# Kernel tuning notes

Hardware: AMD Instinct MI355X
Metric: run time of the kernel (lower is better)

Reference implementation:

```python
import jax, jax.numpy as jnp
import numpy as np

N_NODES = 100000
N_EDGES = 3200000
D_IN = 256
D_OUT = 256


def setup_inputs() -> dict:
    key = jax.random.key(0)
    k1, k2, k3, k4, k5, k6 = jax.random.split(key, 6)
    x = jax.random.normal(k1, (N_NODES, D_IN), dtype=jnp.float32)
    adj_row = jnp.sort(jax.random.randint(k2, (N_EDGES,), 0, N_NODES, dtype=jnp.int64))
    adj_col = jax.random.randint(k3, (N_EDGES,), 0, N_NODES, dtype=jnp.int64)
    adj_val = jax.random.uniform(k4, (N_EDGES,), dtype=jnp.float32)
    stdv = 1.0 / np.sqrt(D_OUT)
    weight = jax.random.uniform(k5, (D_IN, D_OUT), dtype=jnp.float32, minval=-stdv, maxval=stdv)
    bias = jax.random.uniform(k6, (D_OUT,), dtype=jnp.float32, minval=-stdv, maxval=stdv)
    return {"x": x, "adj_row": adj_row, "adj_col": adj_col, "adj_val": adj_val,
            "weight": weight, "bias": bias}


def reference(x, adj_row, adj_col, adj_val, weight, bias):
    # support = x @ W   -> [N, D_OUT]
    support = x @ weight
    # output = spmm(adj, support): gather source rows, scale by edge value,
    # segment-reduce into destination rows.
    msgs = adj_val[:, None] * support[adj_col]          # [E, D_OUT]
    output = jax.ops.segment_sum(msgs, adj_row, num_segments=N_NODES)
    return output + bias
```

## Files before the change

kernel.cpp:

```cpp
#include <hip/hip_runtime.h>
#include <hip/hip_bf16.h>

#define D_FEAT 256

typedef __attribute__((ext_vector_type(8))) __bf16 bf16x8;
typedef __attribute__((ext_vector_type(4))) __bf16 bf16x4;
typedef __attribute__((ext_vector_type(4))) float f32x4;

__global__ __launch_bounds__(256) void cast_wt(
    const float* __restrict__ W, __bf16* __restrict__ Wt) {
  const int n = blockIdx.x;
  const int k = threadIdx.x;
  Wt[n * 256 + k] = (__bf16)W[k * 256 + n];
}

#define APITCH 40

__global__ __launch_bounds__(256) void gemm_mfma(
    const float* __restrict__ X, const __bf16* __restrict__ Wt,
    __bf16* __restrict__ S, int M) {
  __shared__ __bf16 As[128 * APITCH];
  __shared__ __bf16 Bs[64 * APITCH];
  const int tid = threadIdx.x;
  const int wave = tid >> 6;
  const int lane = tid & 63;
  const int m0 = blockIdx.x * 128;
  const int n0 = blockIdx.y * 64;

  f32x4 acc[2][4] = {};

  const int l15 = lane & 15;
  const int kh8 = (lane >> 4) * 8;

  for (int k0 = 0; k0 < D_FEAT; k0 += 32) {
    {
      const int r = tid >> 1;
      const int kh = (tid & 1) * 16;
      const int gr = m0 + r;
      float v[16];
      if (gr < M) {
        const float* src = X + (size_t)gr * D_FEAT + k0 + kh;
#pragma unroll
        for (int q = 0; q < 4; ++q) {
          float4 f = *reinterpret_cast<const float4*>(src + q * 4);
          v[q * 4 + 0] = f.x; v[q * 4 + 1] = f.y;
          v[q * 4 + 2] = f.z; v[q * 4 + 3] = f.w;
        }
      } else {
#pragma unroll
        for (int q = 0; q < 16; ++q) v[q] = 0.f;
      }
      bf16x8 b0, b1;
#pragma unroll
      for (int q = 0; q < 8; ++q) { b0[q] = (__bf16)v[q]; b1[q] = (__bf16)v[q + 8]; }
      *reinterpret_cast<bf16x8*>(&As[r * APITCH + kh]) = b0;
      *reinterpret_cast<bf16x8*>(&As[r * APITCH + kh + 8]) = b1;
    }
    {
      const int nr = tid >> 2;
      const int q = (tid & 3) * 8;
      bf16x8 b = *reinterpret_cast<const bf16x8*>(
          Wt + (size_t)(n0 + nr) * D_FEAT + k0 + q);
      *reinterpret_cast<bf16x8*>(&Bs[nr * APITCH + q]) = b;
    }
    __syncthreads();

    bf16x8 a[2], b[4];
#pragma unroll
    for (int rg = 0; rg < 2; ++rg)
      a[rg] = *reinterpret_cast<const bf16x8*>(
          &As[(wave * 32 + rg * 16 + l15) * APITCH + kh8]);
#pragma unroll
    for (int cg = 0; cg < 4; ++cg)
      b[cg] = *reinterpret_cast<const bf16x8*>(
          &Bs[(cg * 16 + l15) * APITCH + kh8]);
#pragma unroll
    for (int rg = 0; rg < 2; ++rg)
#pragma unroll
      for (int cg = 0; cg < 4; ++cg)
        acc[rg][cg] = __builtin_amdgcn_mfma_f32_16x16x32_bf16(
            a[rg], b[cg], acc[rg][cg], 0, 0, 0);
    __syncthreads();
  }

#pragma unroll
  for (int rg = 0; rg < 2; ++rg) {
    const int rbase = m0 + wave * 32 + rg * 16 + (lane >> 4) * 4;
#pragma unroll
    for (int cg = 0; cg < 4; ++cg) {
      const int c = n0 + cg * 16 + l15;
#pragma unroll
      for (int r = 0; r < 4; ++r) {
        const int row = rbase + r;
        if (row < M) S[(size_t)row * D_FEAT + c] = (__bf16)acc[rg][cg][r];
      }
    }
  }
}

__global__ __launch_bounds__(256) void build_rowptr(
    const int* __restrict__ rows, int E, int* __restrict__ ptr, int N) {
  const int n = blockIdx.x * blockDim.x + threadIdx.x;
  if (n > N) return;
  int lo = 0, hi = E;
  while (lo < hi) {
    const int mid = (lo + hi) >> 1;
    if (rows[mid] < n) lo = mid + 1; else hi = mid;
  }
  ptr[n] = lo;
}

__global__ __launch_bounds__(256) void spmm_rows(
    const __bf16* __restrict__ S, const int* __restrict__ ptr,
    const int* __restrict__ col, const float* __restrict__ val,
    const float* __restrict__ bias, float* __restrict__ out, int N) {
  const int wave = threadIdx.x >> 6;
  const int lane = threadIdx.x & 63;
  const int n = blockIdx.x * 4 + wave;
  if (n >= N) return;

  const int e0 = ptr[n];
  const int e1 = ptr[n + 1];
  const int f0 = lane * 4;

  float a0 = 0.f, a1 = 0.f, a2 = 0.f, a3 = 0.f;
  int e = e0;
  for (; e + 1 < e1; e += 2) {
    const int c0 = col[e];
    const int c1 = col[e + 1];
    const float v0 = val[e];
    const float v1 = val[e + 1];
    bf16x4 s0 = *reinterpret_cast<const bf16x4*>(S + (size_t)c0 * D_FEAT + f0);
    bf16x4 s1 = *reinterpret_cast<const bf16x4*>(S + (size_t)c1 * D_FEAT + f0);
    a0 += v0 * (float)s0[0] + v1 * (float)s1[0];
    a1 += v0 * (float)s0[1] + v1 * (float)s1[1];
    a2 += v0 * (float)s0[2] + v1 * (float)s1[2];
    a3 += v0 * (float)s0[3] + v1 * (float)s1[3];
  }
  if (e < e1) {
    const int c0 = col[e];
    const float v0 = val[e];
    bf16x4 s0 = *reinterpret_cast<const bf16x4*>(S + (size_t)c0 * D_FEAT + f0);
    a0 += v0 * (float)s0[0];
    a1 += v0 * (float)s0[1];
    a2 += v0 * (float)s0[2];
    a3 += v0 * (float)s0[3];
  }
  const float4 b = *reinterpret_cast<const float4*>(bias + f0);
  float4 o = make_float4(a0 + b.x, a1 + b.y, a2 + b.z, a3 + b.w);
  *reinterpret_cast<float4*>(out + (size_t)n * D_FEAT + f0) = o;
}

extern "C" void kernel_launch(void* const* d_in, const int* in_sizes, int n_in,
                              void* d_out, int out_size, void* d_ws, size_t ws_size,
                              hipStream_t stream) {
  const float* x       = (const float*)d_in[0];
  const int*   adj_row = (const int*)d_in[1];
  const int*   adj_col = (const int*)d_in[2];
  const float* adj_val = (const float*)d_in[3];
  const float* weight  = (const float*)d_in[4];
  const float* bias    = (const float*)d_in[5];
  float*       out     = (float*)d_out;

  const int N = in_sizes[0] / D_FEAT;
  const int E = in_sizes[1];

  __bf16* Wt      = (__bf16*)d_ws;
  __bf16* support = Wt + 256 * 256;
  int*    rowptr  = (int*)(support + (size_t)N * D_FEAT);

  cast_wt<<<256, 256, 0, stream>>>(weight, Wt);

  {
    dim3 grid((N + 127) / 128, D_FEAT / 64);
    gemm_mfma<<<grid, 256, 0, stream>>>(x, Wt, support, N);
  }
  {
    const int threads = 256;
    const int blocks = (N + 1 + threads - 1) / threads;
    build_rowptr<<<blocks, threads, 0, stream>>>(adj_row, E, rowptr, N);
  }
  {
    const int blocks = (N + 3) / 4;
    spmm_rows<<<blocks, 256, 0, stream>>>(support, rowptr, adj_col, adj_val,
                                          bias, out, N);
  }
}
```

Baseline: 318.5 us.

## Prefetch X tiles in GEMM, reorder grid, split SpMM edges across half-waves

The GEMM now software-prefetches the next K-slice of X into registers while the current slice is computed. Its grid is also swapped so the four N-tiles of the same row block run adjacently, which improves L2 reuse of X. The SpMM kernel has each half-wave handle alternating edges with 16-byte bf16x8 gathers, combines the halves with a cross-lane shuffle, and writes output with nontemporal stores. These changes target the gather latency and the GEMM load stalls, at the cost of more registers and shuffle overhead.

New measurement: 305.8 us. -4.0%, faster.

```diff
diff --git a/kernel.cpp b/kernel.cpp
--- a/kernel.cpp
+++ b/kernel.cpp
@@ -4,7 +4,6 @@
 #define D_FEAT 256
 
 typedef __attribute__((ext_vector_type(8))) __bf16 bf16x8;
-typedef __attribute__((ext_vector_type(4))) __bf16 bf16x4;
 typedef __attribute__((ext_vector_type(4))) float f32x4;
 
 __global__ __launch_bounds__(256) void cast_wt(
@@ -24,44 +23,52 @@
   const int tid = threadIdx.x;
   const int wave = tid >> 6;
   const int lane = tid & 63;
-  const int m0 = blockIdx.x * 128;
-  const int n0 = blockIdx.y * 64;
+  const int m0 = blockIdx.y * 128;
+  const int n0 = blockIdx.x * 64;
 
   f32x4 acc[2][4] = {};
 
   const int l15 = lane & 15;
   const int kh8 = (lane >> 4) * 8;
 
+  const int r = tid >> 1;
+  const int kh = (tid & 1) * 16;
+  const int gr = m0 + r;
+  const bool valid = gr < M;
+  const float* xsrc = X + (size_t)(valid ? gr : 0) * D_FEAT + kh;
+
+  float4 pre[4];
+#pragma unroll
+  for (int q = 0; q < 4; ++q)
+    pre[q] = valid ? *reinterpret_cast<const float4*>(xsrc + q * 4)
+                   : make_float4(0.f, 0.f, 0.f, 0.f);
+
+  const int nr = tid >> 2;
+  const int q4 = (tid & 3) * 8;
+
   for (int k0 = 0; k0 < D_FEAT; k0 += 32) {
-    {
-      const int r = tid >> 1;
-      const int kh = (tid & 1) * 16;
-      const int gr = m0 + r;
-      float v[16];
-      if (gr < M) {
-        const float* src = X + (size_t)gr * D_FEAT + k0 + kh;
-#pragma unroll
-        for (int q = 0; q < 4; ++q) {
-          float4 f = *reinterpret_cast<const float4*>(src + q * 4);
-          v[q * 4 + 0] = f.x; v[q * 4 + 1] = f.y;
-          v[q * 4 + 2] = f.z; v[q * 4 + 3] = f.w;
-        }
-      } else {
-#pragma unroll
-        for (int q = 0; q < 16; ++q) v[q] = 0.f;
-      }
-      bf16x8 b0, b1;
-#pragma unroll
-      for (int q = 0; q < 8; ++q) { b0[q] = (__bf16)v[q]; b1[q] = (__bf16)v[q + 8]; }
-      *reinterpret_cast<bf16x8*>(&As[r * APITCH + kh]) = b0;
-      *reinterpret_cast<bf16x8*>(&As[r * APITCH + kh + 8]) = b1;
-    }
-    {
-      const int nr = tid >> 2;
-      const int q = (tid & 3) * 8;
-      bf16x8 b = *reinterpret_cast<const bf16x8*>(
-          Wt + (size_t)(n0 + nr) * D_FEAT + k0 + q);
-      *reinterpret_cast<bf16x8*>(&Bs[nr * APITCH + q]) = b;
+    bf16x8 wb = *reinterpret_cast<const bf16x8*>(
+        Wt + (size_t)(n0 + nr) * D_FEAT + k0 + q4);
+
+    bf16x8 a0, a1;
+    a0[0] = (__bf16)pre[0].x; a0[1] = (__bf16)pre[0].y;
+    a0[2] = (__bf16)pre[0].z; a0[3] = (__bf16)pre[0].w;
+    a0[4] = (__bf16)pre[1].x; a0[5] = (__bf16)pre[1].y;
+    a0[6] = (__bf16)pre[1].z; a0[7] = (__bf16)pre[1].w;
+    a1[0] = (__bf16)pre[2].x; a1[1] = (__bf16)pre[2].y;
+    a1[2] = (__bf16)pre[2].z; a1[3] = (__bf16)pre[2].w;
+    a1[4] = (__bf16)pre[3].x; a1[5] = (__bf16)pre[3].y;
+    a1[6] = (__bf16)pre[3].z; a1[7] = (__bf16)pre[3].w;
+    *reinterpret_cast<bf16x8*>(&As[r * APITCH + kh]) = a0;
+    *reinterpret_cast<bf16x8*>(&As[r * APITCH + kh + 8]) = a1;
+    *reinterpret_cast<bf16x8*>(&Bs[nr * APITCH + q4]) = wb;
+
+    const bool have = (k0 + 32) < D_FEAT;
+    float4 nxt[4];
+    if (have && valid) {
+#pragma unroll
+      for (int q = 0; q < 4; ++q)
+        nxt[q] = *reinterpret_cast<const float4*>(xsrc + k0 + 32 + q * 4);
     }
     __syncthreads();
 
@@ -81,6 +88,11 @@
         acc[rg][cg] = __builtin_amdgcn_mfma_f32_16x16x32_bf16(
             a[rg], b[cg], acc[rg][cg], 0, 0, 0);
     __syncthreads();
+
+    if (have && valid) {
+#pragma unroll
+      for (int q = 0; q < 4; ++q) pre[q] = nxt[q];
+    }
   }
 
 #pragma unroll
@@ -90,9 +102,9 @@
     for (int cg = 0; cg < 4; ++cg) {
       const int c = n0 + cg * 16 + l15;
 #pragma unroll
-      for (int r = 0; r < 4; ++r) {
-        const int row = rbase + r;
-        if (row < M) S[(size_t)row * D_FEAT + c] = (__bf16)acc[rg][cg][r];
+      for (int rr = 0; rr < 4; ++rr) {
+        const int row = rbase + rr;
+        if (row < M) S[(size_t)row * D_FEAT + c] = (__bf16)acc[rg][cg][rr];
       }
     }
   }
@@ -121,34 +133,38 @@
 
   const int e0 = ptr[n];
   const int e1 = ptr[n + 1];
-  const int f0 = lane * 4;
-
-  float a0 = 0.f, a1 = 0.f, a2 = 0.f, a3 = 0.f;
-  int e = e0;
-  for (; e + 1 < e1; e += 2) {
-    const int c0 = col[e];
-    const int c1 = col[e + 1];
-    const float v0 = val[e];
-    const float v1 = val[e + 1];
-    bf16x4 s0 = *reinterpret_cast<const bf16x4*>(S + (size_t)c0 * D_FEAT + f0);
-    bf16x4 s1 = *reinterpret_cast<const bf16x4*>(S + (size_t)c1 * D_FEAT + f0);
-    a0 += v0 * (float)s0[0] + v1 * (float)s1[0];
-    a1 += v0 * (float)s0[1] + v1 * (float)s1[1];
-    a2 += v0 * (float)s0[2] + v1 * (float)s1[2];
-    a3 += v0 * (float)s0[3] + v1 * (float)s1[3];
-  }
-  if (e < e1) {
-    const int c0 = col[e];
-    const float v0 = val[e];
-    bf16x4 s0 = *reinterpret_cast<const bf16x4*>(S + (size_t)c0 * D_FEAT + f0);
-    a0 += v0 * (float)s0[0];
-    a1 += v0 * (float)s0[1];
-    a2 += v0 * (float)s0[2];
-    a3 += v0 * (float)s0[3];
-  }
-  const float4 b = *reinterpret_cast<const float4*>(bias + f0);
-  float4 o = make_float4(a0 + b.x, a1 + b.y, a2 + b.z, a3 + b.w);
-  *reinterpret_cast<float4*>(out + (size_t)n * D_FEAT + f0) = o;
+  const int hw = lane >> 5;
+  const int l5 = lane & 31;
+  const int f0 = l5 * 8;
+
+  float acc[8] = {};
+  const int deg = e1 - e0;
+  const int nit = (deg + 1) >> 1;
+
+#pragma unroll 4
+  for (int it = 0; it < nit; ++it) {
+    const int e = e0 + 2 * it + hw;
+    int c = 0;
+    float v = 0.f;
+    if (e < e1) { c = col[e]; v = val[e]; }
+    bf16x8 s = *reinterpret_cast<const bf16x8*>(S + (size_t)c * D_FEAT + f0);
+#pragma unroll
+    for (int j = 0; j < 8; ++j) acc[j] += v * (float)s[j];
+  }
+
+#pragma unroll
+  for (int j = 0; j < 8; ++j) acc[j] += __shfl(acc[j], lane ^ 32, 64);
+
+  const int fw = f0 + hw * 4;
+  const float4 b = *reinterpret_cast<const float4*>(bias + fw);
+  const float r0 = hw ? acc[4] : acc[0];
+  const float r1 = hw ? acc[5] : acc[1];
+  const float r2 = hw ? acc[6] : acc[2];
+  const float r3 = hw ? acc[7] : acc[3];
+  f32x4 o;
+  o[0] = r0 + b.x; o[1] = r1 + b.y; o[2] = r2 + b.z; o[3] = r3 + b.w;
+  __builtin_nontemporal_store(
+      o, reinterpret_cast<f32x4*>(out + (size_t)n * D_FEAT + fw));
 }
 
 extern "C" void kernel_launch(void* const* d_in, const int* in_sizes, int n_in,
@@ -172,7 +188,7 @@
   cast_wt<<<256, 256, 0, stream>>>(weight, Wt);
 
   {
-    dim3 grid((N + 127) / 128, D_FEAT / 64);
+    dim3 grid(D_FEAT / 64, (N + 127) / 128);
     gemm_mfma<<<grid, 256, 0, stream>>>(x, Wt, support, N);
   }
   {
```
